# Performance work log

Hardware: AMD Instinct MI355X
Metric: run time of the kernel (lower is better)

## Reference

```python
import jax, jax.numpy as jnp
import numpy as np

EMBED_DIM = 1024
NUM_HEADS = 16
HEAD_DIM = EMBED_DIM // NUM_HEADS


def setup_inputs() -> dict:
    key = jax.random.key(0)
    k_x, k_qw, k_qb, k_ow, k_ob = jax.random.split(key, 5)
    B, T, C = 2, 2048, EMBED_DIM
    scale = 1.0 / np.sqrt(C)
    return {
        "x": jax.random.normal(k_x, (B, T, C), dtype=jnp.float32),
        "qkv_w": jax.random.normal(k_qw, (C, 3 * C), dtype=jnp.float32) * scale,
        "qkv_b": jax.random.normal(k_qb, (3 * C,), dtype=jnp.float32) * 0.02,
        "out_w": jax.random.normal(k_ow, (C, C), dtype=jnp.float32) * scale,
        "out_b": jax.random.normal(k_ob, (C,), dtype=jnp.float32) * 0.02,
    }


def reference(x, qkv_w, qkv_b, out_w, out_b):
    # x: (B, T, C). Causal masked multi-head self-attention (eval mode: dropout off).
    B, T, C = x.shape
    H, Dh = NUM_HEADS, HEAD_DIM
    qkv = x @ qkv_w + qkv_b                      # (B, T, 3C)
    qkv = qkv.reshape(B, T, 3, H, Dh)
    q = jnp.transpose(qkv[:, :, 0], (0, 2, 1, 3))  # (B, H, T, Dh)
    k = jnp.transpose(qkv[:, :, 1], (0, 2, 1, 3))
    v = jnp.transpose(qkv[:, :, 2], (0, 2, 1, 3))
    scores = jnp.einsum("bhqd,bhkd->bhqk", q, k) / np.sqrt(Dh)
    causal = jnp.tril(jnp.ones((T, T), dtype=bool))
    scores = jnp.where(causal[None, None], scores, -jnp.inf)
    attn = jax.nn.softmax(scores, axis=-1)        # (B, H, T, T)
    out = jnp.einsum("bhqk,bhkd->bhqd", attn, v)  # (B, H, T, Dh)
    out = jnp.transpose(out, (0, 2, 1, 3)).reshape(B, T, C)
    return out @ out_w + out_b
```

## Files before the change

### kernel.cpp

```cpp
#include <hip/hip_runtime.h>


typedef __bf16 bf16;
typedef __attribute__((ext_vector_type(4))) __bf16 bf16x4;
typedef __attribute__((ext_vector_type(8))) __bf16 bf16x8;
typedef __attribute__((ext_vector_type(4))) float f32x4;

#define T_SEQ 2048
#define NHEAD 16
#define QSCALE 0.1803368801111244f

__device__ __forceinline__ void async16(const bf16* g, const bf16* l) {
    __builtin_amdgcn_global_load_lds(
        (const __attribute__((address_space(1))) void*)g,
        (__attribute__((address_space(3))) void*)l, 16, 0, 0);
}

__global__ __launch_bounds__(256) void prep(
    const float* __restrict__ x, bf16* __restrict__ xb,
    const float* __restrict__ qkv_w, bf16* __restrict__ wbT,
    const float* __restrict__ out_w, bf16* __restrict__ owbT) {
    const int bid = blockIdx.x, tid = threadIdx.x;
    if (bid < 4096) {
        int i = (bid * 256 + tid) * 4;
        float4 v = *(const float4*)(x + i);
        bf16x4 o;
        o.x = (bf16)v.x; o.y = (bf16)v.y; o.z = (bf16)v.z; o.w = (bf16)v.w;
        *(bf16x4*)(xb + i) = o;
        return;
    }
    __shared__ float tile[32][33];
    const float* in;
    bf16* out;
    int K_, N_, b;
    if (bid < 7168) { b = bid - 4096; in = qkv_w; out = wbT; K_ = 1024; N_ = 3072; }
    else            { b = bid - 7168; in = out_w; out = owbT; K_ = 1024; N_ = 1024; }
    int k0 = (b & 31) * 32, n0 = (b >> 5) * 32;
    int tx = tid & 31, ty = tid >> 5;
    for (int r = 0; r < 32; r += 8)
        tile[ty + r][tx] = in[(k0 + ty + r) * N_ + n0 + tx];
    __syncthreads();
    for (int r = 0; r < 32; r += 8)
        out[(n0 + ty + r) * K_ + k0 + tx] = (bf16)tile[tx][ty + r];
}

__global__ __launch_bounds__(256) void gemm_qkv(
    const bf16* __restrict__ A, const bf16* __restrict__ Bt,
    const float* __restrict__ bias,
    bf16* __restrict__ Qo, bf16* __restrict__ Ko, bf16* __restrict__ Vt) {
    __shared__ __align__(16) bf16 As[128 * 32];
    __shared__ __align__(16) bf16 Bs[128 * 32];
    const int t = threadIdx.x;
    const int lane = t & 63, wave = t >> 6;
    const int l15 = lane & 15, quad = lane >> 4;
    const int wm = wave & 1, wn = wave >> 1;
    const int m0 = blockIdx.y * 128, n0 = blockIdx.x * 128;
    const int sec = n0 >> 10;

    f32x4 acc[4][4] = {};

    const int sfat = t >> 3, sp = t & 7;
    const int slg = sp ^ (sfat & 7);
    const int smrow = sfat * 2 + (slg >> 2);
    const int skoff = (slg & 3) << 3;
    const bf16* ag = A + (m0 + smrow) * 1024 + skoff;
    const bf16* bg = Bt + (n0 + smrow) * 1024 + skoff;
    bf16* as0 = As + wave * 512;
    bf16* as1 = As + 2048 + wave * 512;
    bf16* bs0 = Bs + wave * 512;
    bf16* bs1 = Bs + 2048 + wave * 512;

    const int foff = (l15 >> 1) * 64 + (((((l15 & 1) << 2) | quad)) ^ (l15 >> 1)) * 8;

    if (sec < 2) {
        for (int k0 = 0; k0 < 1024; k0 += 32) {
            async16(ag + k0, as0);
            async16(ag + 64 * 1024 + k0, as1);
            async16(bg + k0, bs0);
            async16(bg + 64 * 1024 + k0, bs1);
            __syncthreads();
            bf16x8 af[4], bfr[4];
            for (int i = 0; i < 4; i++)
                af[i] = *(const bf16x8*)(As + (wm * 64 + i * 16) * 32 + foff);
            for (int j = 0; j < 4; j++)
                bfr[j] = *(const bf16x8*)(Bs + (wn * 64 + j * 16) * 32 + foff);
            for (int j = 0; j < 4; j++)
                for (int i = 0; i < 4; i++)
                    acc[j][i] = __builtin_amdgcn_mfma_f32_16x16x32_bf16(bfr[j], af[i], acc[j][i], 0, 0, 0);
            __syncthreads();
        }
        bf16* dst = (sec == 0) ? Qo : Ko;
        const float sc = (sec == 0) ? QSCALE : 1.0f;
        for (int j = 0; j < 4; j++) {
            int col0 = n0 + wn * 64 + j * 16 + quad * 4;
            float4 bv = *(const float4*)(bias + col0);
            int c2 = col0 & 1023, h = c2 >> 6, d0 = c2 & 63;
            for (int i = 0; i < 4; i++) {
                int row = m0 + wm * 64 + i * 16 + l15;
                int b = row >> 11, tt = row & 2047;
                int bh = b * NHEAD + h;
                bf16x4 o;
                o[0] = (bf16)((acc[j][i][0] + bv.x) * sc);
                o[1] = (bf16)((acc[j][i][1] + bv.y) * sc);
                o[2] = (bf16)((acc[j][i][2] + bv.z) * sc);
                o[3] = (bf16)((acc[j][i][3] + bv.w) * sc);
                *(bf16x4*)(dst + (bh * T_SEQ + tt) * 64 + d0) = o;
            }
        }
    } else {
        for (int k0 = 0; k0 < 1024; k0 += 32) {
            async16(ag + k0, as0);
            async16(ag + 64 * 1024 + k0, as1);
            async16(bg + k0, bs0);
            async16(bg + 64 * 1024 + k0, bs1);
            __syncthreads();
            bf16x8 af[4], bfr[4];
            for (int i = 0; i < 4; i++)
                af[i] = *(const bf16x8*)(As + (wm * 64 + i * 16) * 32 + foff);
            for (int j = 0; j < 4; j++)
                bfr[j] = *(const bf16x8*)(Bs + (wn * 64 + j * 16) * 32 + foff);
            for (int i = 0; i < 4; i++)
                for (int j = 0; j < 4; j++)
                    acc[i][j] = __builtin_amdgcn_mfma_f32_16x16x32_bf16(af[i], bfr[j], acc[i][j], 0, 0, 0);
            __syncthreads();
        }
        for (int j = 0; j < 4; j++) {
            int col = n0 + wn * 64 + j * 16 + l15;
            float bv = bias[col];
            int c2 = col & 1023, h = c2 >> 6, d = c2 & 63;
            for (int i = 0; i < 4; i++) {
                int row0 = m0 + wm * 64 + i * 16 + quad * 4;
                int b = row0 >> 11, tt0 = row0 & 2047;
                int bh = b * NHEAD + h;
                bf16x4 o;
                for (int r = 0; r < 4; r++)
                    o[r] = (bf16)(acc[i][j][r] + bv);
                *(bf16x4*)(Vt + (bh * 64 + d) * T_SEQ + tt0) = o;
            }
        }
    }
}

#define PST 80
__global__ __launch_bounds__(256, 4) void attn(
    const bf16* __restrict__ Q, const bf16* __restrict__ K,
    const bf16* __restrict__ Vt, bf16* __restrict__ AO) {
    __shared__ __align__(16) bf16 Ks[2][64 * 64];
    __shared__ __align__(16) bf16 Vs[2][64 * 64];
    __shared__ __align__(16) bf16 Pa[4][16 * PST];
    const int tid = threadIdx.x;
    const int lane = tid & 63, wave = tid >> 6;
    const int l15 = lane & 15, quad = lane >> 4;
    const int xcdr = blockIdx.x & 7;
    const int i_ = blockIdx.x >> 3;
    const int bh = (xcdr << 2) | (i_ & 3);
    const int ti = i_ >> 2;
    const int qt = (ti & 1) ? (ti >> 1) : (31 - (ti >> 1));
    const int t0w = qt * 64 + wave * 16;

    const bf16* kp = K + bh * T_SEQ * 64;
    const bf16* vp = Vt + bh * 64 * T_SEQ;
    bf16* pw = &Pa[wave][0];
    const int b_ = bh >> 4, h_ = bh & 15;

    const int sx = (quad ^ (l15 & 7)) << 3;

    const bf16* qp = Q + (bh * T_SEQ + t0w) * 64;
    bf16x8 qf0 = *(const bf16x8*)(qp + l15 * 64 + quad * 8);
    bf16x8 qf1 = *(const bf16x8*)(qp + l15 * 64 + 32 + quad * 8);

    auto stage = [&](int kb, int b) {
        for (int i = 0; i < 2; i++) {
            int row = i * 32 + (tid >> 3), p = tid & 7;
            const bf16* ksrc = kp + (kb + row) * 64 + ((p ^ (row & 7)) << 3);
            async16(ksrc, &Ks[b][i * 2048 + wave * 512]);
            const bf16* vsrc = vp + row * T_SEQ + kb + ((p ^ (row & 7)) << 3);
            async16(vsrc, &Vs[b][i * 2048 + wave * 512]);
        }
    };

    f32x4 acc[4] = {};
    float lsum = 0.0f;

    const int C = qt + 1;
    stage(0, 0);
    for (int c = 0; c < C; c++) {
        __syncthreads();
        if (c + 1 < C) stage((c + 1) * 64, (c + 1) & 1);
        const bf16* ksb = &Ks[c & 1][0];
        const bf16* vsb = &Vs[c & 1][0];
        const bool dg = (c == qt);
        const int na = dg ? (wave + 1) : 4;

        f32x4 sc[4];
        for (int n = 0; n < 4; n++) {
            if (n < na) {
                const bf16* kbase = ksb + (n * 16 + l15) * 64;
                bf16x8 kf0 = *(const bf16x8*)(kbase + sx);
                bf16x8 kf1 = *(const bf16x8*)(kbase + (sx ^ 32));
                f32x4 z = {};
                z = __builtin_amdgcn_mfma_f32_16x16x32_bf16(kf0, qf0, z, 0, 0, 0);
                z = __builtin_amdgcn_mfma_f32_16x16x32_bf16(kf1, qf1, z, 0, 0, 0);
                sc[n] = z;
            }
        }
        for (int n = 0; n < 4; n++) {
            bf16x4 pv;
            if (n < na) {
                const bool dmask = dg && (n == na - 1);
                for (int r = 0; r < 4; r++) {
                    float v = sc[n][r];
                    if (dmask && (quad * 4 + r > l15)) v = -100000.0f;
                    float e = __builtin_amdgcn_exp2f(v);
                    lsum += e;
                    pv[r] = (bf16)e;
                }
            } else {
                pv[0] = pv[1] = pv[2] = pv[3] = (bf16)0.0f;
            }
            *(bf16x4*)(pw + l15 * PST + n * 16 + quad * 4) = pv;
        }
        __builtin_amdgcn_s_waitcnt(0xC07F);
        for (int g = 0; g < 2; g++) {
            bf16x8 pf = *(const bf16x8*)(pw + l15 * PST + g * 32 + quad * 8);
            for (int j = 0; j < 4; j++) {
                const bf16* vbase = vsb + (j * 16 + l15) * 64;
                bf16x8 vf = *(const bf16x8*)(vbase + (g ? (sx ^ 32) : sx));
                acc[j] = __builtin_amdgcn_mfma_f32_16x16x32_bf16(pf, vf, acc[j], 0, 0, 0);
            }
        }
    }

    lsum += __shfl_xor(lsum, 16);
    lsum += __shfl_xor(lsum, 32);
    float linv = 1.0f / lsum;

    bf16* aop = AO + (b_ * T_SEQ + t0w) * 1024 + h_ * 64;
    for (int r = 0; r < 4; r++) {
        float lr = __shfl(linv, quad * 4 + r, 16);
        for (int j = 0; j < 4; j++)
            aop[(quad * 4 + r) * 1024 + j * 16 + l15] = (bf16)(acc[j][r] * lr);
    }
}

__global__ __launch_bounds__(256) void gemm_out_k(
    const bf16* __restrict__ A, const bf16* __restrict__ Bt,
    const float* __restrict__ bias, float* __restrict__ out) {
    __shared__ __align__(16) bf16 As[64 * 32];
    __shared__ __align__(16) bf16 Bs[128 * 32];
    const int t = threadIdx.x;
    const int lane = t & 63, wave = t >> 6;
    const int l15 = lane & 15, quad = lane >> 4;
    const int wm = wave & 1, wn = wave >> 1;
    const int m0 = blockIdx.y * 64, n0 = blockIdx.x * 128;

    f32x4 acc[4][2] = {};

    const int sfat = t >> 3, sp = t & 7;
    const int slg = sp ^ (sfat & 7);
    const int smrow = sfat * 2 + (slg >> 2);
    const int skoff = (slg & 3) << 3;
    const bf16* ag = A + (m0 + smrow) * 1024 + skoff;
    const bf16* bg = Bt + (n0 + smrow) * 1024 + skoff;
    bf16* as0 = As + wave * 512;
    bf16* bs0 = Bs + wave * 512;
    bf16* bs1 = Bs + 2048 + wave * 512;

    const int foff = (l15 >> 1) * 64 + (((((l15 & 1) << 2) | quad)) ^ (l15 >> 1)) * 8;

    for (int k0 = 0; k0 < 1024; k0 += 32) {
        async16(ag + k0, as0);
        async16(bg + k0, bs0);
        async16(bg + 64 * 1024 + k0, bs1);
        __syncthreads();
        bf16x8 af[2], bfr[4];
        for (int i = 0; i < 2; i++)
            af[i] = *(const bf16x8*)(As + (wm * 32 + i * 16) * 32 + foff);
        for (int j = 0; j < 4; j++)
            bfr[j] = *(const bf16x8*)(Bs + (wn * 64 + j * 16) * 32 + foff);
        for (int j = 0; j < 4; j++)
            for (int i = 0; i < 2; i++)
                acc[j][i] = __builtin_amdgcn_mfma_f32_16x16x32_bf16(bfr[j], af[i], acc[j][i], 0, 0, 0);
        __syncthreads();
    }

    for (int j = 0; j < 4; j++) {
        int col0 = n0 + wn * 64 + j * 16 + quad * 4;
        float4 bv = *(const float4*)(bias + col0);
        for (int i = 0; i < 2; i++) {
            int row = m0 + wm * 32 + i * 16 + l15;
            float4 o;
            o.x = acc[j][i][0] + bv.x;
            o.y = acc[j][i][1] + bv.y;
            o.z = acc[j][i][2] + bv.z;
            o.w = acc[j][i][3] + bv.w;
            *(float4*)(out + row * 1024 + col0) = o;
        }
    }
}

extern "C" void kernel_launch(void* const* d_in, const int* in_sizes, int n_in,
                              void* d_out, int out_size, void* d_ws, size_t ws_size,
                              hipStream_t stream) {
    const float* x     = (const float*)d_in[0];
    const float* qkv_w = (const float*)d_in[1];
    const float* qkv_b = (const float*)d_in[2];
    const float* out_w = (const float*)d_in[3];
    const float* out_b = (const float*)d_in[4];
    float* out = (float*)d_out;

    char* ws = (char*)d_ws;
    bf16* xb   = (bf16*)(ws);
    bf16* wbT  = (bf16*)(ws + (8ull << 20));
    bf16* owbT = (bf16*)(ws + (14ull << 20));
    bf16* Qb   = (bf16*)(ws + (16ull << 20));
    bf16* Kb   = (bf16*)(ws + (24ull << 20));
    bf16* Vt   = (bf16*)(ws + (32ull << 20));
    bf16* AO   = (bf16*)(ws + (40ull << 20));

    prep<<<8192, 256, 0, stream>>>(x, xb, qkv_w, wbT, out_w, owbT);
    gemm_qkv<<<dim3(24, 32), 256, 0, stream>>>(xb, wbT, qkv_b, Qb, Kb, Vt);
    attn<<<1024, 256, 0, stream>>>(Qb, Kb, Vt, AO);
    gemm_out_k<<<dim3(8, 64), 256, 0, stream>>>(AO, owbT, out_b, out);
}
```

Measured before the change: 175.7 us.

## Rewrite QKV GEMM with 256x256 tiles, double-buffered LDS, interleaved MFMA schedule

The QKV projection GEMM moves from 128x128 tiles with 256 threads and a single-buffered K=32 step to 256x256 tiles with 512 threads and double-buffered K=64 stages. The async global-to-LDS load for the next stage is issued while the current stage's MFMAs run, with s_barrier fences and setprio splitting the compute into four quadrant phases. The aim is to hide load latency, raise arithmetic intensity per LDS byte and halve the number of block-wide syncs. The cost is more LDS (128KB per block) and registers, and only 192 blocks, which may underfill the 256 CUs.

```diff
diff --git a/kernel.cpp b/kernel.cpp
--- a/kernel.cpp
+++ b/kernel.cpp
@@ -44,97 +44,164 @@
         out[(n0 + ty + r) * K_ + k0 + tx] = (bf16)tile[tx][ty + r];
 }
 
-__global__ __launch_bounds__(256) void gemm_qkv(
+#define FENCE_BAR asm volatile("s_barrier" ::: "memory")
+
+#define LOAD_A(MH)                                                        \
+    _Pragma("unroll") for (int ii = 0; ii < 4; ii++) {                    \
+        const bf16* ap = ab + ((MH) * 64 + ii * 16) * 64;                 \
+        afrag[ii][0] = *(const bf16x8*)(ap + g0);                         \
+        afrag[ii][1] = *(const bf16x8*)(ap + g1);                         \
+    }
+#define LOAD_B(NH)                                                        \
+    _Pragma("unroll") for (int jj = 0; jj < 2; jj++) {                    \
+        const bf16* bp = bb + ((NH) * 32 + jj * 16) * 64;                 \
+        bfrag[jj][0] = *(const bf16x8*)(bp + g0);                         \
+        bfrag[jj][1] = *(const bf16x8*)(bp + g1);                         \
+    }
+#define MFMA_SWAP(MH, NH)                                                 \
+    __builtin_amdgcn_s_setprio(1);                                        \
+    _Pragma("unroll") for (int jj = 0; jj < 2; jj++)                      \
+    _Pragma("unroll") for (int ii = 0; ii < 4; ii++)                      \
+    _Pragma("unroll") for (int s = 0; s < 2; s++)                         \
+        acc[(MH) * 4 + ii][(NH) * 2 + jj] =                               \
+            __builtin_amdgcn_mfma_f32_16x16x32_bf16(                      \
+                bfrag[jj][s], afrag[ii][s],                               \
+                acc[(MH) * 4 + ii][(NH) * 2 + jj], 0, 0, 0);              \
+    __builtin_amdgcn_s_setprio(0);
+#define MFMA_NORM(MH, NH)                                                 \
+    __builtin_amdgcn_s_setprio(1);                                        \
+    _Pragma("unroll") for (int ii = 0; ii < 4; ii++)                      \
+    _Pragma("unroll") for (int jj = 0; jj < 2; jj++)                      \
+    _Pragma("unroll") for (int s = 0; s < 2; s++)                         \
+        acc[(MH) * 4 + ii][(NH) * 2 + jj] =                               \
+            __builtin_amdgcn_mfma_f32_16x16x32_bf16(                      \
+                afrag[ii][s], bfrag[jj][s],                               \
+                acc[(MH) * 4 + ii][(NH) * 2 + jj], 0, 0, 0);              \
+    __builtin_amdgcn_s_setprio(0);
+
+__global__ __launch_bounds__(512, 2) void gemm_qkv(
     const bf16* __restrict__ A, const bf16* __restrict__ Bt,
     const float* __restrict__ bias,
     bf16* __restrict__ Qo, bf16* __restrict__ Ko, bf16* __restrict__ Vt) {
-    __shared__ __align__(16) bf16 As[128 * 32];
-    __shared__ __align__(16) bf16 Bs[128 * 32];
+    __shared__ __align__(16) bf16 As[2][256 * 64];
+    __shared__ __align__(16) bf16 Bs[2][256 * 64];
     const int t = threadIdx.x;
     const int lane = t & 63, wave = t >> 6;
     const int l15 = lane & 15, quad = lane >> 4;
-    const int wm = wave & 1, wn = wave >> 1;
-    const int m0 = blockIdx.y * 128, n0 = blockIdx.x * 128;
+    const int wm = wave >> 2, wn = wave & 3;
+    const int m0 = blockIdx.y * 256, n0 = blockIdx.x * 256;
     const int sec = n0 >> 10;
 
-    f32x4 acc[4][4] = {};
-
-    const int sfat = t >> 3, sp = t & 7;
-    const int slg = sp ^ (sfat & 7);
-    const int smrow = sfat * 2 + (slg >> 2);
-    const int skoff = (slg & 3) << 3;
-    const bf16* ag = A + (m0 + smrow) * 1024 + skoff;
-    const bf16* bg = Bt + (n0 + smrow) * 1024 + skoff;
-    bf16* as0 = As + wave * 512;
-    bf16* as1 = As + 2048 + wave * 512;
-    bf16* bs0 = Bs + wave * 512;
-    bf16* bs1 = Bs + 2048 + wave * 512;
-
-    const int foff = (l15 >> 1) * 64 + (((((l15 & 1) << 2) | quad)) ^ (l15 >> 1)) * 8;
+    f32x4 acc[8][4] = {};
+
+    const int srow8 = lane >> 3;
+    const int sgr = (lane & 7) ^ srow8;
+    const bf16* agbase = A + (m0 + wave * 8 + srow8) * 1024 + sgr * 8;
+    const bf16* bgbase = Bt + (n0 + wave * 8 + srow8) * 1024 + sgr * 8;
+
+    auto stage = [&](int buf, int k0) {
+        const bf16* a = agbase + k0;
+        const bf16* b = bgbase + k0;
+        const bf16* as = &As[buf][wave * 512];
+        const bf16* bs = &Bs[buf][wave * 512];
+        async16(a, as);
+        async16(a + 64 * 1024, as + 64 * 64);
+        async16(a + 128 * 1024, as + 128 * 64);
+        async16(a + 192 * 1024, as + 192 * 64);
+        async16(b, bs);
+        async16(b + 64 * 1024, bs + 64 * 64);
+        async16(b + 128 * 1024, bs + 128 * 64);
+        async16(b + 192 * 1024, bs + 192 * 64);
+    };
+
+    const int rsw = l15 & 7;
+    const int g0 = ((0 + quad) ^ rsw) << 3;
+    const int g1 = ((4 + quad) ^ rsw) << 3;
+
+    stage(0, 0);
+    __syncthreads();
 
     if (sec < 2) {
-        for (int k0 = 0; k0 < 1024; k0 += 32) {
-            async16(ag + k0, as0);
-            async16(ag + 64 * 1024 + k0, as1);
-            async16(bg + k0, bs0);
-            async16(bg + 64 * 1024 + k0, bs1);
-            __syncthreads();
-            bf16x8 af[4], bfr[4];
-            for (int i = 0; i < 4; i++)
-                af[i] = *(const bf16x8*)(As + (wm * 64 + i * 16) * 32 + foff);
-            for (int j = 0; j < 4; j++)
-                bfr[j] = *(const bf16x8*)(Bs + (wn * 64 + j * 16) * 32 + foff);
-            for (int j = 0; j < 4; j++)
-                for (int i = 0; i < 4; i++)
-                    acc[j][i] = __builtin_amdgcn_mfma_f32_16x16x32_bf16(bfr[j], af[i], acc[j][i], 0, 0, 0);
+#pragma unroll 2
+        for (int ct = 0; ct < 16; ct++) {
+            const int c = ct & 1;
+            const bf16* ab = &As[c][0] + (wm * 128 + l15) * 64;
+            const bf16* bb = &Bs[c][0] + (wn * 64 + l15) * 64;
+            bf16x8 afrag[4][2], bfrag[2][2];
+            LOAD_A(0);
+            LOAD_B(0);
+            if (ct < 15) stage(c ^ 1, (ct + 1) * 64);
+            FENCE_BAR;
+            MFMA_SWAP(0, 0);
+            FENCE_BAR;
+            LOAD_B(1);
+            FENCE_BAR;
+            MFMA_SWAP(0, 1);
+            FENCE_BAR;
+            LOAD_A(1);
+            FENCE_BAR;
+            MFMA_SWAP(1, 1);
+            FENCE_BAR;
+            LOAD_B(0);
+            FENCE_BAR;
+            MFMA_SWAP(1, 0);
             __syncthreads();
         }
         bf16* dst = (sec == 0) ? Qo : Ko;
         const float sc = (sec == 0) ? QSCALE : 1.0f;
-        for (int j = 0; j < 4; j++) {
-            int col0 = n0 + wn * 64 + j * 16 + quad * 4;
+        for (int nj = 0; nj < 4; nj++) {
+            int col0 = n0 + wn * 64 + nj * 16 + quad * 4;
             float4 bv = *(const float4*)(bias + col0);
             int c2 = col0 & 1023, h = c2 >> 6, d0 = c2 & 63;
-            for (int i = 0; i < 4; i++) {
-                int row = m0 + wm * 64 + i * 16 + l15;
+            for (int mi = 0; mi < 8; mi++) {
+                int row = m0 + wm * 128 + mi * 16 + l15;
                 int b = row >> 11, tt = row & 2047;
                 int bh = b * NHEAD + h;
                 bf16x4 o;
-                o[0] = (bf16)((acc[j][i][0] + bv.x) * sc);
-                o[1] = (bf16)((acc[j][i][1] + bv.y) * sc);
-                o[2] = (bf16)((acc[j][i][2] + bv.z) * sc);
-                o[3] = (bf16)((acc[j][i][3] + bv.w) * sc);
+                o[0] = (bf16)((acc[mi][nj][0] + bv.x) * sc);
+                o[1] = (bf16)((acc[mi][nj][1] + bv.y) * sc);
+                o[2] = (bf16)((acc[mi][nj][2] + bv.z) * sc);
+                o[3] = (bf16)((acc[mi][nj][3] + bv.w) * sc);
                 *(bf16x4*)(dst + (bh * T_SEQ + tt) * 64 + d0) = o;
             }
         }
     } else {
-        for (int k0 = 0; k0 < 1024; k0 += 32) {
-            async16(ag + k0, as0);
-            async16(ag + 64 * 1024 + k0, as1);
-            async16(bg + k0, bs0);
-            async16(bg + 64 * 1024 + k0, bs1);
+#pragma unroll 2
+        for (int ct = 0; ct < 16; ct++) {
+            const int c = ct & 1;
+            const bf16* ab = &As[c][0] + (wm * 128 + l15) * 64;
+            const bf16* bb = &Bs[c][0] + (wn * 64 + l15) * 64;
+            bf16x8 afrag[4][2], bfrag[2][2];
+            LOAD_A(0);
+            LOAD_B(0);
+            if (ct < 15) stage(c ^ 1, (ct + 1) * 64);
+            FENCE_BAR;
+            MFMA_NORM(0, 0);
+            FENCE_BAR;
+            LOAD_B(1);
+            FENCE_BAR;
+            MFMA_NORM(0, 1);
+            FENCE_BAR;
+            LOAD_A(1);
+            FENCE_BAR;
+            MFMA_NORM(1, 1);
+            FENCE_BAR;
+            LOAD_B(0);
+            FENCE_BAR;
+            MFMA_NORM(1, 0);
             __syncthreads();
-            bf16x8 af[4], bfr[4];
-            for (int i = 0; i < 4; i++)
-                af[i] = *(const bf16x8*)(As + (wm * 64 + i * 16) * 32 + foff);
-            for (int j = 0; j < 4; j++)
-                bfr[j] = *(const bf16x8*)(Bs + (wn * 64 + j * 16) * 32 + foff);
-            for (int i = 0; i < 4; i++)
-                for (int j = 0; j < 4; j++)
-                    acc[i][j] = __builtin_amdgcn_mfma_f32_16x16x32_bf16(af[i], bfr[j], acc[i][j], 0, 0, 0);
-            __syncthreads();
-        }
-        for (int j = 0; j < 4; j++) {
-            int col = n0 + wn * 64 + j * 16 + l15;
+        }
+        for (int nj = 0; nj < 4; nj++) {
+            int col = n0 + wn * 64 + nj * 16 + l15;
             float bv = bias[col];
             int c2 = col & 1023, h = c2 >> 6, d = c2 & 63;
-            for (int i = 0; i < 4; i++) {
-                int row0 = m0 + wm * 64 + i * 16 + quad * 4;
+            for (int mi = 0; mi < 8; mi++) {
+                int row0 = m0 + wm * 128 + mi * 16 + quad * 4;
                 int b = row0 >> 11, tt0 = row0 & 2047;
                 int bh = b * NHEAD + h;
                 bf16x4 o;
                 for (int r = 0; r < 4; r++)
-                    o[r] = (bf16)(acc[i][j][r] + bv);
+                    o[r] = (bf16)(acc[mi][nj][r] + bv);
                 *(bf16x4*)(Vt + (bh * 64 + d) * T_SEQ + tt0) = o;
             }
         }
@@ -319,7 +386,7 @@
     bf16* AO   = (bf16*)(ws + (40ull << 20));
 
     prep<<<8192, 256, 0, stream>>>(x, xb, qkv_w, wbT, out_w, owbT);
-    gemm_qkv<<<dim3(24, 32), 256, 0, stream>>>(xb, wbT, qkv_b, Qb, Kb, Vt);
+    gemm_qkv<<<dim3(12, 16), 512, 0, stream>>>(xb, wbT, qkv_b, Qb, Kb, Vt);
     attn<<<1024, 256, 0, stream>>>(Qb, Kb, Vt, AO);
     gemm_out_k<<<dim3(8, 64), 256, 0, stream>>>(AO, owbT, out_b, out);
 }
```

Result: no change. 178.8 us (+1.8%).
